# Kernel tuning notes

Measured on AMD Instinct MI355X. Metric: run time of the kernel, lower is better.

The kernel has to match this reference:

```python
import jax, jax.numpy as jnp
import numpy as np

MAX_SEQ_LEN = 2048
ADJ_SCALE = 0.1


def setup_inputs() -> dict:
    key = jax.random.key(0)
    k1, k2, k3 = jax.random.split(key, 3)
    B, L, H, D = 8, 2048, 16, 64
    x = jax.random.normal(k1, (B, L, H, D), dtype=jnp.float32)
    W = jax.random.normal(k2, (D, D), dtype=jnp.float32) * (1.0 / np.sqrt(D))
    b = jax.random.normal(k3, (D,), dtype=jnp.float32) * 0.02
    gate = jnp.ones((1,), dtype=jnp.float32) * 0.5  # betweenness_gate init
    return {"x": x, "W": W, "b": b, "gate": gate}


def reference(x, W, b, gate):
    B, L, H, D = x.shape
    # --- RoPE frequency table (precompute_freqs_cis) ---
    base_freqs = 1.0 / (10000.0 ** (jnp.arange(0, D, 2, dtype=jnp.float32) / D))  # (D/2,)
    t = jnp.arange(L, dtype=jnp.float32)
    freqs = t[:, None] * base_freqs[None, :]          # (L, D/2)
    fcos, fsin = jnp.cos(freqs), jnp.sin(freqs)

    # --- betweenness: only consecutive-pair distances are ever used ---
    content = jnp.einsum('blhd,ed->blhe', x, W) + b    # nn.Linear(dim, dim)
    d1 = jnp.linalg.norm(content[:, 1:] - content[:, :-1], axis=-1)   # (B, L-1, H)  d(i, i+1)
    d2 = jnp.linalg.norm(content[:, 2:] - content[:, :-2], axis=-1)   # (B, L-2, H)  d(i, i+2)
    direct = d2
    path = d1[:, :-1] + d1[:, 1:]
    score = jax.nn.relu(1.0 - (path - direct) / jnp.maximum(direct, 1e-6))  # (B, L-2, H)
    betweenness = jnp.zeros((B, L, H), x.dtype).at[:, 1:L - 1].set(score / (L - 2))

    # --- betweenness-adjusted interpolated RoPE (vectorized over positions) ---
    adjust = gate[0] * (betweenness - 0.5) * ADJ_SCALE               # (B, L, H)
    pos = jnp.arange(L, dtype=jnp.float32)[None, :, None]
    adj_pos = jnp.clip(pos + adjust, 0.0, MAX_SEQ_LEN - 1)
    lo = jnp.floor(adj_pos).astype(jnp.int32)
    hi = jnp.ceil(adj_pos).astype(jnp.int32)
    frac = (adj_pos - lo)[..., None]                                 # (B, L, H, 1)
    cos_i = (1.0 - frac) * fcos[lo] + frac * fcos[hi]                # (B, L, H, D/2)
    sin_i = (1.0 - frac) * fsin[lo] + frac * fsin[hi]

    x_even = x[..., 0::2]
    x_odd = x[..., 1::2]
    out_even = x_even * cos_i - x_odd * sin_i
    out_odd = x_odd * cos_i + x_even * sin_i
    out = jnp.stack([out_even, out_odd], axis=-1).reshape(B, L, H, D)  # re-interleave
    return out
```

## Files before the change

kernel.cpp:

```cpp
#include <hip/hip_runtime.h>

#define L_SEQ 2048
#define HEADS 16
#define DIM   64
#define TILE  32
#define XROWS 34
#define XPITCH 68
#define DROWS 48

typedef __attribute__((ext_vector_type(8))) short bf16x8;
typedef __attribute__((ext_vector_type(4))) float f32x4;
typedef __attribute__((ext_vector_type(8))) unsigned short u16x8;

static __device__ __forceinline__ unsigned short f2bf(float f) {
    unsigned int u = __builtin_bit_cast(unsigned int, f);
    u += 0x7fffu + ((u >> 16) & 1u);
    return (unsigned short)(u >> 16);
}

#define SWZ(row, col) ((row) * 64 + ((col) ^ (((row) & 7) * 8)))

__global__ void prep_w_kernel(const float* __restrict__ W, unsigned short* __restrict__ wbf) {
    int i = blockIdx.x * 256 + threadIdx.x;
    if (i < DIM * DIM) wbf[i] = f2bf(W[i]);
}

__global__ __launch_bounds__(256) void betweenness_rope_kernel(
    const float* __restrict__ x, const float* __restrict__ W,
    const unsigned short* __restrict__ wbf, const float* __restrict__ gate,
    float* __restrict__ out)
{
    __shared__ float xs[XROWS * XPITCH];
    __shared__ unsigned short dl[DROWS * 64];
    __shared__ float n1s[34];
    __shared__ float g1s[33];
    __shared__ float2 fl[32];

    const int tid  = threadIdx.x;
    const int lane = tid & 63;
    const int wave = tid >> 6;
    const int la   = lane & 15, lg = lane >> 4;
    const int l0   = blockIdx.x * TILE;
    const int h    = blockIdx.y;
    const int b    = blockIdx.z;
    const int bh_off = (b * L_SEQ * HEADS + h) * DIM;

    for (int c = tid; c < XROWS * 16; c += 256) {
        int r = c >> 4, q = c & 15;
        int g = l0 - 1 + r; g = max(0, min(L_SEQ - 1, g));
        float4 v = *(const float4*)(x + bh_off + g * (HEADS * DIM) + q * 4);
        *(float4*)&xs[r * XPITCH + q * 4] = v;
    }
    __syncthreads();

    for (int r = tid >> 3; r < DROWS; r += 32) {
        int c0 = (tid & 7) * 8;
        u16x8 o = {0, 0, 0, 0, 0, 0, 0, 0};
        if (r <= 32) {
            float4 a0 = *(float4*)&xs[r * XPITCH + c0];
            float4 a1 = *(float4*)&xs[r * XPITCH + c0 + 4];
            float4 b0 = *(float4*)&xs[(r + 1) * XPITCH + c0];
            float4 b1 = *(float4*)&xs[(r + 1) * XPITCH + c0 + 4];
            o[0] = f2bf(b0.x - a0.x); o[1] = f2bf(b0.y - a0.y);
            o[2] = f2bf(b0.z - a0.z); o[3] = f2bf(b0.w - a0.w);
            o[4] = f2bf(b1.x - a1.x); o[5] = f2bf(b1.y - a1.y);
            o[6] = f2bf(b1.z - a1.z); o[7] = f2bf(b1.w - a1.w);
        }
        *(u16x8*)&dl[SWZ(r, c0)] = o;
    }
    __syncthreads();

    {
        bf16x8 bfrag[2];
        const int n = 16 * wave + la;
        if (wbf) {
            bfrag[0] = *(const bf16x8*)(wbf + n * 64 + lg * 8);
            bfrag[1] = *(const bf16x8*)(wbf + n * 64 + lg * 8 + 32);
        } else {
            #pragma unroll
            for (int kt = 0; kt < 2; ++kt) {
                const float* wr = W + n * 64 + lg * 8 + kt * 32;
                float4 w0 = *(const float4*)(wr);
                float4 w1 = *(const float4*)(wr + 4);
                u16x8 t = { f2bf(w0.x), f2bf(w0.y), f2bf(w0.z), f2bf(w0.w),
                            f2bf(w1.x), f2bf(w1.y), f2bf(w1.z), f2bf(w1.w) };
                bfrag[kt] = __builtin_bit_cast(bf16x8, t);
            }
        }
        bf16x8 afrag[3][2];
        #pragma unroll
        for (int mt = 0; mt < 3; ++mt)
            #pragma unroll
            for (int kt = 0; kt < 2; ++kt)
                afrag[mt][kt] = *(const bf16x8*)&dl[SWZ(16 * mt + la, lg * 8 + kt * 32)];
        f32x4 acc[3];
        #pragma unroll
        for (int mt = 0; mt < 3; ++mt) {
            f32x4 a_ = {0.f, 0.f, 0.f, 0.f};
            a_ = __builtin_amdgcn_mfma_f32_16x16x32_bf16(afrag[mt][0], bfrag[0], a_, 0, 0, 0);
            a_ = __builtin_amdgcn_mfma_f32_16x16x32_bf16(afrag[mt][1], bfrag[1], a_, 0, 0, 0);
            acc[mt] = a_;
        }
        __syncthreads();
        #pragma unroll
        for (int mt = 0; mt < 3; ++mt)
            #pragma unroll
            for (int q = 0; q < 4; ++q)
                dl[SWZ(16 * mt + lg * 4 + q, 16 * wave + la)] = f2bf(acc[mt][q]);
    }
    __syncthreads();

    {
        const int ntile = (wave == 0) ? 2 : 1;
        for (int s = 0; s < ntile; ++s) {
            int t = (s == 0) ? wave : 4;
            int mt = (t < 3) ? t : ((t == 3) ? 0 : 1);
            int nt = (t < 3) ? t : ((t == 3) ? 1 : 2);
            f32x4 g = {0.f, 0.f, 0.f, 0.f};
            #pragma unroll
            for (int kt = 0; kt < 2; ++kt) {
                int cb = lg * 8 + kt * 32;
                bf16x8 a  = *(const bf16x8*)&dl[SWZ(16 * mt + la, cb)];
                bf16x8 bb = *(const bf16x8*)&dl[SWZ(16 * nt + la, cb)];
                g = __builtin_amdgcn_mfma_f32_16x16x32_bf16(a, bb, g, 0, 0, 0);
            }
            #pragma unroll
            for (int q = 0; q < 4; ++q) {
                int R = 16 * mt + lg * 4 + q, C = 16 * nt + la;
                if (C == R && R < 34) n1s[R] = g[q];
                if (C == R + 1 && R < 33) g1s[R] = g[q];
            }
        }
    }
    __syncthreads();

    if (tid < 32) {
        const float gate0 = gate[0];
        int r = tid, l = l0 + r;
        float a1 = n1s[r], b1 = n1s[r + 1], gg = g1s[r];
        float d1a = sqrtf(a1), d1b = sqrtf(b1);
        float dd  = sqrtf(fmaxf(a1 + b1 + 2.f * gg, 0.f));
        float sc  = fmaxf(1.f - ((d1a + d1b) - dd) / fmaxf(dd, 1e-6f), 0.f);
        float bet = (l >= 1 && l <= L_SEQ - 2) ? sc * (1.f / (L_SEQ - 2)) : 0.f;
        float adjust = gate0 * (bet - 0.5f) * 0.1f;
        float ap  = fminf(fmaxf((float)l + adjust, 0.f), (float)(L_SEQ - 1));
        float flo = floorf(ap);
        fl[r] = make_float2(flo, ap - flo);
    }
    __syncthreads();

    {
        const int j = lane & 31, half = lane >> 5;
        const float fjr = __builtin_exp2f(-0.4152410118609203f * (float)j)
                        * 0.15915494309189535f;
        const float cf = __builtin_amdgcn_cosf(fjr);
        const float sf = __builtin_amdgcn_sinf(fjr);
        const float cfm1 = cf - 1.0f;
        const int r0w = wave * 2 + half;
        const float* xbase = &xs[(r0w + 1) * XPITCH + 2 * j];
        float* obase = out + bh_off + (l0 + r0w) * (HEADS * DIM) + 2 * j;
        #pragma unroll
        for (int it = 0; it < 4; ++it) {
            int r = it * 8 + r0w;
            float2 ff = fl[r];
            float t0 = ff.x * fjr;
            float rv = t0 - floorf(t0);
            float c_lo = __builtin_amdgcn_cosf(rv);
            float s_lo = __builtin_amdgcn_sinf(rv);
            float u = fmaf(ff.y, cfm1, 1.0f);
            float v = ff.y * sf;
            float ci = fmaf(-s_lo, v, c_lo * u);
            float si = fmaf(c_lo, v, s_lo * u);
            float2 xv = *(const float2*)(xbase + it * 8 * XPITCH);
            float2 o;
            o.x = xv.x * ci - xv.y * si;
            o.y = fmaf(xv.y, ci, xv.x * si);
            *(float2*)(obase + it * 8 * (HEADS * DIM)) = o;
        }
    }
}

extern "C" void kernel_launch(void* const* d_in, const int* in_sizes, int n_in,
                              void* d_out, int out_size, void* d_ws, size_t ws_size,
                              hipStream_t stream) {
    const float* x    = (const float*)d_in[0];
    const float* W    = (const float*)d_in[1];
    const float* gate = (const float*)d_in[3];
    float* out = (float*)d_out;

    const int B = in_sizes[0] / (L_SEQ * HEADS * DIM);

    unsigned short* wbf = nullptr;
    if (ws_size >= (size_t)(DIM * DIM * sizeof(unsigned short))) {
        wbf = (unsigned short*)d_ws;
        prep_w_kernel<<<16, 256, 0, stream>>>(W, wbf);
    }

    dim3 grid(L_SEQ / TILE, HEADS, B);
    betweenness_rope_kernel<<<grid, 256, 0, stream>>>(x, W, wbf, gate, out);
}
```

Measured before the change: 40.12 us.

## Double sequence tile to 64 rows with 512 threads and separate GEMM output buffer

Raises the per-block sequence tile from 32 to 64 positions and the block size from 256 to 512 threads. This halves the halo overhead and the number of blocks. The content GEMM now writes into a separate LDS buffer, which removes a barrier, and its work is split into 20 per-wave 16x16 jobs. Float-to-bf16 conversion switches to a perm-based truncating pack instead of round-to-nearest-even, which slightly changes numerical accuracy. Larger blocks use more LDS and may reduce occupancy or grid parallelism.

```diff
diff --git a/kernel.cpp b/kernel.cpp
--- a/kernel.cpp
+++ b/kernel.cpp
@@ -3,38 +3,57 @@
 #define L_SEQ 2048
 #define HEADS 16
 #define DIM   64
-#define TILE  32
-#define XROWS 34
+#define TILE  64
+#define XROWS 66
 #define XPITCH 68
-#define DROWS 48
+#define DROWS 80
 
 typedef __attribute__((ext_vector_type(8))) short bf16x8;
 typedef __attribute__((ext_vector_type(4))) float f32x4;
-typedef __attribute__((ext_vector_type(8))) unsigned short u16x8;
 
-static __device__ __forceinline__ unsigned short f2bf(float f) {
+static __device__ __forceinline__ unsigned short f2bf_rtne(float f) {
     unsigned int u = __builtin_bit_cast(unsigned int, f);
     u += 0x7fffu + ((u >> 16) & 1u);
     return (unsigned short)(u >> 16);
+}
+static __device__ __forceinline__ unsigned int pk2(float a, float b) {
+    return __builtin_amdgcn_perm(__builtin_bit_cast(unsigned int, b),
+                                 __builtin_bit_cast(unsigned int, a), 0x07060302u);
+}
+static __device__ __forceinline__ unsigned short f2bf_trunc(float f) {
+    return (unsigned short)(__builtin_bit_cast(unsigned int, f) >> 16);
 }
 
 #define SWZ(row, col) ((row) * 64 + ((col) ^ (((row) & 7) * 8)))
 
 __global__ void prep_w_kernel(const float* __restrict__ W, unsigned short* __restrict__ wbf) {
     int i = blockIdx.x * 256 + threadIdx.x;
-    if (i < DIM * DIM) wbf[i] = f2bf(W[i]);
+    if (i < DIM * DIM) wbf[i] = f2bf_rtne(W[i]);
 }
 
-__global__ __launch_bounds__(256) void betweenness_rope_kernel(
+static __device__ __forceinline__ bf16x8 load_bfrag(const unsigned short* wbf,
+                                                    const float* W, int n, int k0) {
+    if (wbf) return *(const bf16x8*)(wbf + n * 64 + k0);
+    const float* wr = W + n * 64 + k0;
+    float4 w0 = *(const float4*)wr;
+    float4 w1 = *(const float4*)(wr + 4);
+    uint4 p;
+    p.x = pk2(w0.x, w0.y); p.y = pk2(w0.z, w0.w);
+    p.z = pk2(w1.x, w1.y); p.w = pk2(w1.z, w1.w);
+    return __builtin_bit_cast(bf16x8, p);
+}
+
+__global__ __launch_bounds__(512) void betweenness_rope_kernel(
     const float* __restrict__ x, const float* __restrict__ W,
     const unsigned short* __restrict__ wbf, const float* __restrict__ gate,
     float* __restrict__ out)
 {
     __shared__ float xs[XROWS * XPITCH];
     __shared__ unsigned short dl[DROWS * 64];
-    __shared__ float n1s[34];
-    __shared__ float g1s[33];
-    __shared__ float2 fl[32];
+    __shared__ unsigned short el[DROWS * 64];
+    __shared__ float n1s[65];
+    __shared__ float g1s[64];
+    __shared__ float2 fl[TILE];
 
     const int tid  = threadIdx.x;
     const int lane = tid & 63;
@@ -45,7 +64,7 @@
     const int b    = blockIdx.z;
     const int bh_off = (b * L_SEQ * HEADS + h) * DIM;
 
-    for (int c = tid; c < XROWS * 16; c += 256) {
+    for (int c = tid; c < XROWS * 16; c += 512) {
         int r = c >> 4, q = c & 15;
         int g = l0 - 1 + r; g = max(0, min(L_SEQ - 1, g));
         float4 v = *(const float4*)(x + bh_off + g * (HEADS * DIM) + q * 4);
@@ -53,88 +72,59 @@
     }
     __syncthreads();
 
-    for (int r = tid >> 3; r < DROWS; r += 32) {
-        int c0 = (tid & 7) * 8;
-        u16x8 o = {0, 0, 0, 0, 0, 0, 0, 0};
-        if (r <= 32) {
+    for (int c = tid; c < DROWS * 8; c += 512) {
+        int r = c >> 3, c0 = (c & 7) * 8;
+        uint4 o = {0u, 0u, 0u, 0u};
+        if (r <= 64) {
             float4 a0 = *(float4*)&xs[r * XPITCH + c0];
             float4 a1 = *(float4*)&xs[r * XPITCH + c0 + 4];
             float4 b0 = *(float4*)&xs[(r + 1) * XPITCH + c0];
             float4 b1 = *(float4*)&xs[(r + 1) * XPITCH + c0 + 4];
-            o[0] = f2bf(b0.x - a0.x); o[1] = f2bf(b0.y - a0.y);
-            o[2] = f2bf(b0.z - a0.z); o[3] = f2bf(b0.w - a0.w);
-            o[4] = f2bf(b1.x - a1.x); o[5] = f2bf(b1.y - a1.y);
-            o[6] = f2bf(b1.z - a1.z); o[7] = f2bf(b1.w - a1.w);
+            o.x = pk2(b0.x - a0.x, b0.y - a0.y);
+            o.y = pk2(b0.z - a0.z, b0.w - a0.w);
+            o.z = pk2(b1.x - a1.x, b1.y - a1.y);
+            o.w = pk2(b1.z - a1.z, b1.w - a1.w);
         }
-        *(u16x8*)&dl[SWZ(r, c0)] = o;
+        *(uint4*)&dl[SWZ(r, c0)] = o;
     }
     __syncthreads();
 
-    {
-        bf16x8 bfrag[2];
-        const int n = 16 * wave + la;
-        if (wbf) {
-            bfrag[0] = *(const bf16x8*)(wbf + n * 64 + lg * 8);
-            bfrag[1] = *(const bf16x8*)(wbf + n * 64 + lg * 8 + 32);
-        } else {
-            #pragma unroll
-            for (int kt = 0; kt < 2; ++kt) {
-                const float* wr = W + n * 64 + lg * 8 + kt * 32;
-                float4 w0 = *(const float4*)(wr);
-                float4 w1 = *(const float4*)(wr + 4);
-                u16x8 t = { f2bf(w0.x), f2bf(w0.y), f2bf(w0.z), f2bf(w0.w),
-                            f2bf(w1.x), f2bf(w1.y), f2bf(w1.z), f2bf(w1.w) };
-                bfrag[kt] = __builtin_bit_cast(bf16x8, t);
-            }
-        }
-        bf16x8 afrag[3][2];
+    for (int job = wave; job < 20; job += 8) {
+        int mt = job >> 2, nt = job & 3;
+        bf16x8 a0 = *(const bf16x8*)&dl[SWZ(16 * mt + la, lg * 8)];
+        bf16x8 a1 = *(const bf16x8*)&dl[SWZ(16 * mt + la, lg * 8 + 32)];
+        bf16x8 b0 = load_bfrag(wbf, W, 16 * nt + la, lg * 8);
+        bf16x8 b1 = load_bfrag(wbf, W, 16 * nt + la, lg * 8 + 32);
+        f32x4 acc = {0.f, 0.f, 0.f, 0.f};
+        acc = __builtin_amdgcn_mfma_f32_16x16x32_bf16(a0, b0, acc, 0, 0, 0);
+        acc = __builtin_amdgcn_mfma_f32_16x16x32_bf16(a1, b1, acc, 0, 0, 0);
         #pragma unroll
-        for (int mt = 0; mt < 3; ++mt)
-            #pragma unroll
-            for (int kt = 0; kt < 2; ++kt)
-                afrag[mt][kt] = *(const bf16x8*)&dl[SWZ(16 * mt + la, lg * 8 + kt * 32)];
-        f32x4 acc[3];
-        #pragma unroll
-        for (int mt = 0; mt < 3; ++mt) {
-            f32x4 a_ = {0.f, 0.f, 0.f, 0.f};
-            a_ = __builtin_amdgcn_mfma_f32_16x16x32_bf16(afrag[mt][0], bfrag[0], a_, 0, 0, 0);
-            a_ = __builtin_amdgcn_mfma_f32_16x16x32_bf16(afrag[mt][1], bfrag[1], a_, 0, 0, 0);
-            acc[mt] = a_;
-        }
-        __syncthreads();
-        #pragma unroll
-        for (int mt = 0; mt < 3; ++mt)
-            #pragma unroll
-            for (int q = 0; q < 4; ++q)
-                dl[SWZ(16 * mt + lg * 4 + q, 16 * wave + la)] = f2bf(acc[mt][q]);
+        for (int q = 0; q < 4; ++q)
+            el[SWZ(16 * mt + lg * 4 + q, 16 * nt + la)] = f2bf_trunc(acc[q]);
     }
     __syncthreads();
 
-    {
-        const int ntile = (wave == 0) ? 2 : 1;
-        for (int s = 0; s < ntile; ++s) {
-            int t = (s == 0) ? wave : 4;
-            int mt = (t < 3) ? t : ((t == 3) ? 0 : 1);
-            int nt = (t < 3) ? t : ((t == 3) ? 1 : 2);
-            f32x4 g = {0.f, 0.f, 0.f, 0.f};
-            #pragma unroll
-            for (int kt = 0; kt < 2; ++kt) {
-                int cb = lg * 8 + kt * 32;
-                bf16x8 a  = *(const bf16x8*)&dl[SWZ(16 * mt + la, cb)];
-                bf16x8 bb = *(const bf16x8*)&dl[SWZ(16 * nt + la, cb)];
-                g = __builtin_amdgcn_mfma_f32_16x16x32_bf16(a, bb, g, 0, 0, 0);
-            }
-            #pragma unroll
-            for (int q = 0; q < 4; ++q) {
-                int R = 16 * mt + lg * 4 + q, C = 16 * nt + la;
-                if (C == R && R < 34) n1s[R] = g[q];
-                if (C == R + 1 && R < 33) g1s[R] = g[q];
-            }
+    for (int job = wave; job < 9; job += 8) {
+        int mt = (job < 5) ? job : job - 5;
+        int nt = (job < 5) ? job : job - 4;
+        f32x4 g = {0.f, 0.f, 0.f, 0.f};
+        #pragma unroll
+        for (int kt = 0; kt < 2; ++kt) {
+            int cb = lg * 8 + kt * 32;
+            bf16x8 a  = *(const bf16x8*)&el[SWZ(16 * mt + la, cb)];
+            bf16x8 bb = *(const bf16x8*)&el[SWZ(16 * nt + la, cb)];
+            g = __builtin_amdgcn_mfma_f32_16x16x32_bf16(a, bb, g, 0, 0, 0);
+        }
+        #pragma unroll
+        for (int q = 0; q < 4; ++q) {
+            int R = 16 * mt + lg * 4 + q, C = 16 * nt + la;
+            if (C == R && R < 65) n1s[R] = g[q];
+            if (C == R + 1 && R < 64) g1s[R] = g[q];
         }
     }
     __syncthreads();
 
-    if (tid < 32) {
+    if (tid < TILE) {
         const float gate0 = gate[0];
         int r = tid, l = l0 + r;
         float a1 = n1s[r], b1 = n1s[r + 1], gg = g1s[r];
@@ -161,7 +151,7 @@
         float* obase = out + bh_off + (l0 + r0w) * (HEADS * DIM) + 2 * j;
         #pragma unroll
         for (int it = 0; it < 4; ++it) {
-            int r = it * 8 + r0w;
+            int r = it * 16 + r0w;
             float2 ff = fl[r];
             float t0 = ff.x * fjr;
             float rv = t0 - floorf(t0);
@@ -171,11 +161,11 @@
             float v = ff.y * sf;
             float ci = fmaf(-s_lo, v, c_lo * u);
             float si = fmaf(c_lo, v, s_lo * u);
-            float2 xv = *(const float2*)(xbase + it * 8 * XPITCH);
+            float2 xv = *(const float2*)(xbase + it * 16 * XPITCH);
             float2 o;
             o.x = xv.x * ci - xv.y * si;
             o.y = fmaf(xv.y, ci, xv.x * si);
-            *(float2*)(obase + it * 8 * (HEADS * DIM)) = o;
+            *(float2*)(obase + it * 16 * (HEADS * DIM)) = o;
         }
     }
 }
@@ -197,5 +187,5 @@
     }
 
     dim3 grid(L_SEQ / TILE, HEADS, B);
-    betweenness_rope_kernel<<<grid, 256, 0, stream>>>(x, W, wbf, gate, out);
+    betweenness_rope_kernel<<<grid, 512, 0, stream>>>(x, W, wbf, gate, out);
 }
```

New measurement: 47.26 us. 1.18x slower.
